# Optimization experiments

Measured on AMD Instinct MI355X. Metric: run time of the kernel, lower is better.

Reference implementation:

```python
import jax, jax.numpy as jnp
import numpy as np

D_MODEL = 1024; D_STATE = 64; D_CONV = 7; EXPAND = 2; HEADDIM = 64; NGROUPS = 1
D_INNER = EXPAND * D_MODEL            # 2048
NHEADS = D_INNER // HEADDIM           # 32
D_IN_PROJ = 2 * D_INNER + 2 * (2 * NGROUPS * D_STATE) + 2 * NHEADS  # 4416
CONV_DIM = D_INNER + 2 * (2 * NGROUPS * D_STATE)                     # 2304
BATCH = 2; SEQLEN = 2048
EPS = 1e-5


def setup_inputs() -> dict:
    key = jax.random.key(0)
    ks = jax.random.split(key, 8)
    u = jax.random.normal(ks[0], (BATCH, SEQLEN, D_MODEL), jnp.float32)
    W_in = jax.random.normal(ks[1], (D_IN_PROJ, D_MODEL), jnp.float32) * 0.02
    conv_w = jax.random.normal(ks[2], (CONV_DIM, 1, D_CONV), jnp.float32) * 0.2
    conv_b = jax.random.normal(ks[3], (CONV_DIM,), jnp.float32) * 0.02
    # dt_bias init as in module: inv-softplus of dt sampled log-uniform in [dt_min, dt_max]
    dt = jnp.exp(jax.random.uniform(ks[4], (NHEADS,)) * (np.log(0.1) - np.log(0.001)) + np.log(0.001))
    dt = jnp.clip(dt, 1e-4)
    dt_bias = dt + jnp.log(-jnp.expm1(-dt))
    A_log = jnp.zeros((NHEADS,), jnp.float32)          # A = -exp(A_log) = -1
    Dp = jnp.ones((NHEADS,), jnp.float32)
    fc_D_w = jax.random.normal(ks[5], (NHEADS, D_INNER), jnp.float32) * 0.02
    norm_w = jnp.ones((D_INNER,), jnp.float32)
    W_out = jax.random.normal(ks[6], (D_MODEL, D_INNER), jnp.float32) * 0.02
    return dict(u=u, W_in=W_in, conv_w=conv_w, conv_b=conv_b, dt_bias=dt_bias,
                A_log=A_log, Dp=Dp, fc_D_w=fc_D_w, norm_w=norm_w, W_out=W_out)


def reference(u, W_in, conv_w, conv_b, dt_bias, A_log, Dp, fc_D_w, norm_w, W_out):
    b, L, _ = u.shape
    gn = NGROUPS * D_STATE
    zxbcdt = jnp.einsum('bld,ed->ble', u, W_in)              # (b,L,4416)
    A = -jnp.exp(A_log)                                       # (H,)
    z = zxbcdt[..., :D_INNER]
    xBC = zxbcdt[..., D_INNER:D_INNER + CONV_DIM]
    dt_raw = zxbcdt[..., D_INNER + CONV_DIM:]                 # (b,L,2H)
    # fwd dt + time-flipped bwd dt stacked along batch -> (2b,L,H)
    dt = jnp.concatenate([dt_raw[..., :NHEADS], dt_raw[..., NHEADS:][:, ::-1]], axis=0)
    dt = jax.nn.softplus(dt + dt_bias)                        # dt_limit=(0,inf): softplus already >= 0
    # depthwise conv1d, 'same' padding
    xc = jnp.transpose(xBC, (0, 2, 1))                        # (b,Cd,L)
    xc = jax.lax.conv_general_dilated(xc, conv_w, (1,), [(D_CONV // 2, D_CONV // 2)],
                                      dimension_numbers=('NCH', 'OIH', 'NCH'),
                                      feature_group_count=CONV_DIM)
    xc = xc + conv_b[None, :, None]
    xBC = jax.nn.silu(jnp.transpose(xc, (0, 2, 1)))           # (b,L,Cd)
    x = xBC[..., :D_INNER]
    BC = xBC[..., D_INNER:]
    x_og = x
    x2 = jnp.concatenate([x, x[:, ::-1]], axis=0)             # (2b,L,d_inner)
    BC2 = jnp.concatenate([BC[..., :2 * gn], BC[..., 2 * gn:][:, ::-1]], axis=0)
    Bm = BC2[..., :gn].reshape(2 * b, L, NGROUPS, D_STATE)
    Cm = BC2[..., gn:].reshape(2 * b, L, NGROUPS, D_STATE)
    x_scan = x2.reshape(2 * b, L, NHEADS, HEADDIM)
    hpg = NHEADS // NGROUPS
    Bh = jnp.repeat(Bm, hpg, axis=2)                          # (2b,L,H,N)
    Ch = jnp.repeat(Cm, hpg, axis=2)

    def step(state, ins):                                     # state: (2b,H,P,N)
        x_t, dt_t, B_t, C_t = ins
        ex = jnp.exp(A[None, :, None, None] * dt_t[:, :, None, None])
        state = state * ex + x_t[..., None] * B_t[:, :, None, :]
        y_t = jnp.sum(state * C_t[:, :, None, :], axis=-1)    # (2b,H,P)
        return state, y_t

    xs = (jnp.moveaxis(x_scan, 1, 0), jnp.moveaxis(dt, 1, 0),
          jnp.moveaxis(Bh, 1, 0), jnp.moveaxis(Ch, 1, 0))
    state0 = jnp.zeros((2 * b, NHEADS, HEADDIM, D_STATE), u.dtype)
    _, ys = jax.lax.scan(step, state0, xs)                    # (L,2b,H,P)
    y = jnp.moveaxis(ys, 0, 1).reshape(2 * b, L, D_INNER)
    # shift_right: drop last step, zero at t=0
    y = jnp.concatenate([jnp.zeros_like(y[:, :1]), y[:, :-1]], axis=1)
    y_fw, y_bw = y[:b], y[b:][:, ::-1]
    diag_heads = jnp.einsum('bld,hd->blh', x_og, fc_D_w) + Dp # fc_D(x_og) with bias D
    diag = jnp.repeat(diag_heads, HEADDIM, axis=-1)           # expand per-head -> d_inner
    y = y_fw + y_bw + x_og * diag
    # RMSNormGated (norm before gate)
    rms = jnp.sqrt(jnp.mean(y * y, axis=-1, keepdims=True) + EPS)
    y = norm_w * (y / rms) * jax.nn.silu(z)
    return jnp.einsum('ble,de->bld', y, W_out)
```

## Files before the change

kernel.cpp:

```cpp
#include <hip/hip_runtime.h>
#include <cstdint>
#include <cstddef>

#define L_SEQ   2048
#define DMODEL  1024
#define DINNER  2048
#define NHEADS_ 32
#define HEADDIM_ 64
#define DSTATE  64
#define CONVDIM 2304
#define DINPROJ 4416
#define DINPROJ_P 4480
#define BATCH_  2
#define EPS_    1e-5f
#define PITCH   72
#define KSPL    8

typedef __attribute__((ext_vector_type(8))) short bf16x8;
typedef __attribute__((ext_vector_type(4))) float f32x4;
typedef unsigned short ushort_t;
typedef unsigned int uint_t;
typedef __attribute__((address_space(3))) unsigned int as3_uint;
typedef __attribute__((address_space(1))) const unsigned int as1_uint;

__device__ __forceinline__ float silu_f(float v) { return v / (1.f + __expf(-v)); }
__device__ __forceinline__ ushort_t f2bf(float f) {
    uint_t u = __float_as_uint(f);
    return (ushort_t)((u + 0x7FFFu + ((u >> 16) & 1u)) >> 16);
}
__device__ __forceinline__ float bf2f(ushort_t u) {
    return __uint_as_float(((uint_t)u) << 16);
}
__device__ __forceinline__ void gload16(const void* g, void* l) {
    __builtin_amdgcn_global_load_lds((as1_uint*)g, (as3_uint*)l, 16, 0, 0);
}

__global__ __launch_bounds__(256)
void cvt_bf16(const float* __restrict__ src, ushort_t* __restrict__ dst) {
    const size_t i4 = (size_t)blockIdx.x * 256 + threadIdx.x;
    float4 v = reinterpret_cast<const float4*>(src)[i4];
    ushort_t* d = dst + i4 * 4;
    d[0] = f2bf(v.x); d[1] = f2bf(v.y); d[2] = f2bf(v.z); d[3] = f2bf(v.w);
}

__global__ __launch_bounds__(256)
void cvt_bf16_pad(const float* __restrict__ src, ushort_t* __restrict__ dst) {
    const size_t i4 = (size_t)blockIdx.x * 256 + threadIdx.x;
    const int row = (int)(i4 / (DMODEL / 4));
    float4 v = make_float4(0.f, 0.f, 0.f, 0.f);
    if (row < DINPROJ) v = reinterpret_cast<const float4*>(src)[i4];
    ushort_t* d = dst + i4 * 4;
    d[0] = f2bf(v.x); d[1] = f2bf(v.y); d[2] = f2bf(v.z); d[3] = f2bf(v.w);
}

__global__ __launch_bounds__(256)
void cvt_fcd(const float* __restrict__ src, ushort_t* __restrict__ dst) {
    const size_t i4 = (size_t)blockIdx.x * 256 + threadIdx.x;
    const int row = (int)(i4 / (DINNER / 4));
    float4 v = make_float4(0.f, 0.f, 0.f, 0.f);
    if (row < NHEADS_) v = reinterpret_cast<const float4*>(src)[i4];
    ushort_t* d = dst + i4 * 4;
    d[0] = f2bf(v.x); d[1] = f2bf(v.y); d[2] = f2bf(v.z); d[3] = f2bf(v.w);
}

template<int BM, int BN, int WGM, int WGN, int FM, int FN, int MODE>
__global__ __launch_bounds__(256)
void gemm_nt_mfma(const ushort_t* __restrict__ A, const ushort_t* __restrict__ B,
                  float* __restrict__ C, ushort_t* __restrict__ Cbf,
                  int M, int N, int K, int lda, int ldb, int nbn) {
    const int nwg = gridDim.x;
    const int orig = blockIdx.x;
    const int xcd = orig & 7, q = nwg >> 3, r = nwg & 7;
    const int wg = ((xcd < r) ? (xcd * (q + 1)) : (r * (q + 1) + (xcd - r) * q)) + (orig >> 3);

    int bm, bn, kbeg, kend, ks = 0;
    if (MODE == 2) {
        bm = (wg / nbn) * BM; bn = 0; ks = wg % nbn;
        kbeg = ks * (K / nbn); kend = kbeg + K / nbn;
    } else {
        bm = (wg / nbn) * BM; bn = (wg % nbn) * BN;
        kbeg = 0; kend = K;
    }

    constexpr int BUFSZ = (BM + BN) * 64;
    constexpr int EPI_B = (MODE == 2) ? 0 : BM * 256;
    constexpr int SMEM_B = (2 * BUFSZ > EPI_B) ? 2 * BUFSZ : EPI_B;
    __shared__ __align__(16) char smem[SMEM_B];

    const int tid = threadIdx.x;
    const int wave = tid >> 6, lane = tid & 63;
    const int wr = wave / WGN, wc = wave % WGN;
    const int fr = lane & 15, kg = lane >> 4;

    constexpr int AI = BM / 64, BI = BN / 64;
    size_t aoff[AI]; int aLds[AI];
#pragma unroll
    for (int pp = 0; pp < AI; ++pp) {
        int p = wave * AI + pp;
        int row = p * 16 + (lane >> 2);
        int c16 = (lane & 3) ^ ((row >> 1) & 3);
        aoff[pp] = (size_t)(bm + row) * lda + c16 * 8;
        aLds[pp] = p * 1024;
    }
    size_t boff[BI]; int bLds[BI];
#pragma unroll
    for (int pp = 0; pp < BI; ++pp) {
        int p = wave * BI + pp;
        int row = p * 16 + (lane >> 2);
        int c16 = (lane & 3) ^ ((row >> 1) & 3);
        boff[pp] = (size_t)(bn + row) * ldb + c16 * 8;
        bLds[pp] = BM * 64 + p * 1024;
    }

    auto stage = [&](int buf, int k0) {
        char* bp = smem + buf * BUFSZ;
#pragma unroll
        for (int pp = 0; pp < AI; ++pp) gload16(&A[aoff[pp] + k0], bp + aLds[pp]);
#pragma unroll
        for (int pp = 0; pp < BI; ++pp) gload16(&B[boff[pp] + k0], bp + bLds[pp]);
    };

    f32x4 acc[FM][FN];
#pragma unroll
    for (int m = 0; m < FM; ++m)
#pragma unroll
        for (int n = 0; n < FN; ++n) acc[m][n] = (f32x4){0.f, 0.f, 0.f, 0.f};

    stage(0, kbeg);
    __syncthreads();

    const int NT = (kend - kbeg) / 32;
    for (int t = 0; t < NT; ++t) {
        const int cur = t & 1;
        if (t + 1 < NT) stage(cur ^ 1, kbeg + (t + 1) * 32);

        const char* bp = smem + cur * BUFSZ;
        bf16x8 af[FM], bfv[FN];
#pragma unroll
        for (int m = 0; m < FM; ++m) {
            int row = wr * FM * 16 + m * 16 + fr;
            af[m] = *reinterpret_cast<const bf16x8*>(bp + row * 64 + ((kg ^ ((row >> 1) & 3)) << 4));
        }
#pragma unroll
        for (int n = 0; n < FN; ++n) {
            int row = wc * FN * 16 + n * 16 + fr;
            bfv[n] = *reinterpret_cast<const bf16x8*>(bp + BM * 64 + row * 64 + ((kg ^ ((row >> 1) & 3)) << 4));
        }
#pragma unroll
        for (int m = 0; m < FM; ++m)
#pragma unroll
            for (int n = 0; n < FN; ++n)
                acc[m][n] = __builtin_amdgcn_mfma_f32_16x16x32_bf16(af[m], bfv[n], acc[m][n], 0, 0, 0);
        __syncthreads();
    }

    const int rg = lane >> 4;
    if (MODE == 2) {
        float* Cp = C + (size_t)ks * M * NHEADS_;
#pragma unroll
        for (int m = 0; m < FM; ++m)
#pragma unroll
            for (int n = 0; n < FN; ++n) {
                int col = wc * FN * 16 + n * 16 + fr;
#pragma unroll
                for (int r = 0; r < 4; ++r) {
                    int rowg = bm + wr * FM * 16 + m * 16 + rg * 4 + r;
                    if (col < NHEADS_) Cp[(size_t)rowg * NHEADS_ + col] = acc[m][n][r];
                }
            }
    } else {
        constexpr int ESZ = (MODE == 1) ? 2 : 4;
        char* ct = smem;
#pragma unroll
        for (int m = 0; m < FM; ++m)
#pragma unroll
            for (int n = 0; n < FN; ++n) {
#pragma unroll
                for (int r = 0; r < 4; ++r) {
                    int lr = wr * FM * 16 + m * 16 + rg * 4 + r;
                    int lc = wc * FN * 16 + n * 16 + fr;
                    int byte = (lr * 256 + lc * ESZ) ^ ((lr & 7) << 4);
                    if (MODE == 1) *reinterpret_cast<ushort_t*>(ct + byte) = f2bf(acc[m][n][r]);
                    else           *reinterpret_cast<float*>(ct + byte) = acc[m][n][r];
                }
            }
        __syncthreads();
        const int lrow = tid >> 4, seg16 = (tid & 15) * 16;
#pragma unroll
        for (int j = 0; j < BM / 16; ++j) {
            int lr = j * 16 + lrow;
            uint4 v = *reinterpret_cast<const uint4*>(ct + ((lr * 256 + seg16) ^ ((lr & 7) << 4)));
            if (MODE == 1)
                *reinterpret_cast<uint4*>(&Cbf[(size_t)(bm + lr) * N + bn + seg16 / 2]) = v;
            else
                *reinterpret_cast<uint4*>(&C[(size_t)(bm + lr) * N + bn + seg16 / 4]) = v;
        }
    }
}

__global__ __launch_bounds__(256)
void conv_kernel(const ushort_t* __restrict__ zxbf, const float* __restrict__ conv_w,
                 const float* __restrict__ conv_b, ushort_t* __restrict__ xBCbf) {
    const int c = blockIdx.x * 256 + threadIdx.x;
    const int t0 = blockIdx.y * 16;
    const int beta = blockIdx.z;
    float w[7];
#pragma unroll
    for (int k = 0; k < 7; ++k) w[k] = conv_w[c * 7 + k];
    const float bias = conv_b[c];
    const ushort_t* in = zxbf + (size_t)beta * L_SEQ * DINPROJ_P + DINNER + c;
    float win[7];
#pragma unroll
    for (int j = 0; j < 6; ++j) {
        int t = t0 - 3 + j;
        win[j] = (t >= 0 && t < L_SEQ) ? bf2f(in[(size_t)t * DINPROJ_P]) : 0.f;
    }
    for (int i = 0; i < 16; ++i) {
        int t = t0 + i;
        int tl = t + 3;
        win[6] = (tl < L_SEQ) ? bf2f(in[(size_t)tl * DINPROJ_P]) : 0.f;
        float acc = bias;
#pragma unroll
        for (int k = 0; k < 7; ++k) acc += win[k] * w[k];
        xBCbf[((size_t)beta * L_SEQ + t) * CONVDIM + c] = f2bf(silu_f(acc));
#pragma unroll
        for (int j = 0; j < 6; ++j) win[j] = win[j + 1];
    }
}

__global__ __launch_bounds__(256)
void dtla_kernel(const ushort_t* __restrict__ zxbf, const float* __restrict__ dt_bias,
                 const float* __restrict__ A_log, float* __restrict__ labuf) {
    const int idx = blockIdx.x * 256 + threadIdx.x;
    const int h   = idx & 31;
    const int tau = (idx >> 5) & (L_SEQ - 1);
    const int bd  = idx >> 16;
    const int dir = bd >> 1, beta = bd & 1;
    const int tt  = dir ? (L_SEQ - 1 - tau) : tau;
    const float dtraw = bf2f(zxbf[((size_t)beta * L_SEQ + tt) * DINPROJ_P + DINNER + CONVDIM + dir * NHEADS_ + h]);
    const float Ah = -__expf(A_log[h]);
    const float dtv = dtraw + dt_bias[h];
    const float sp = (dtv > 15.f) ? dtv : log1pf(__expf(dtv));
    labuf[((size_t)bd * NHEADS_ + h) * L_SEQ + tau] = Ah * sp;
}

__global__ __launch_bounds__(256)
void ssd_chunk_kernel(const ushort_t* __restrict__ xBCbf, const float* __restrict__ labuf,
                      float* __restrict__ Pbuf, float* __restrict__ sdel,
                      ushort_t* __restrict__ yfw, ushort_t* __restrict__ ybw) {
    const int c  = blockIdx.x;
    const int h  = blockIdx.y;
    const int bd = blockIdx.z;
    const int dir = bd >> 1, beta = bd & 1;
    const int tid = threadIdx.x;
    const int wave = tid >> 6, lane = tid & 63;
    const int wr = wave >> 1, wc = wave & 1;
    const int fr = lane & 15, kg = lane >> 4, rg = lane >> 4;

    __shared__ short Bs[64 * PITCH], Cs[64 * PITCH], XTs[64 * PITCH],
                     BTs[64 * PITCH], Ms[64 * PITCH];
    __shared__ float lslds[64];

    const int row = tid >> 2, seg = tid & 3;
    const int tau_r = c * 64 + row;
    const int tt = dir ? (L_SEQ - 1 - tau_r) : tau_r;
    const ushort_t* gbase = xBCbf + ((size_t)beta * L_SEQ + tt) * CONVDIM;

    union U4 { uint4 v; ushort_t s[8]; };
    U4 x0, x1, b0, b1, c0, c1;
    x0.v = *reinterpret_cast<const uint4*>(gbase + h * 64 + seg * 16);
    x1.v = *reinterpret_cast<const uint4*>(gbase + h * 64 + seg * 16 + 8);
    b0.v = *reinterpret_cast<const uint4*>(gbase + DINNER + dir * 128 + seg * 16);
    b1.v = *reinterpret_cast<const uint4*>(gbase + DINNER + dir * 128 + seg * 16 + 8);
    c0.v = *reinterpret_cast<const uint4*>(gbase + DINNER + dir * 128 + 64 + seg * 16);
    c1.v = *reinterpret_cast<const uint4*>(gbase + DINNER + dir * 128 + 64 + seg * 16 + 8);

    *reinterpret_cast<uint4*>(&Bs[row * PITCH + seg * 16])     = b0.v;
    *reinterpret_cast<uint4*>(&Bs[row * PITCH + seg * 16 + 8]) = b1.v;
    *reinterpret_cast<uint4*>(&Cs[row * PITCH + seg * 16])     = c0.v;
    *reinterpret_cast<uint4*>(&Cs[row * PITCH + seg * 16 + 8]) = c1.v;
#pragma unroll
    for (int k = 0; k < 8; ++k) {
        XTs[(seg * 16 + k) * PITCH + row]     = x0.s[k];
        XTs[(seg * 16 + 8 + k) * PITCH + row] = x1.s[k];
    }

    if (tid < 64) {
        float v = labuf[((size_t)bd * NHEADS_ + h) * L_SEQ + c * 64 + tid];
#pragma unroll
        for (int d = 1; d < 64; d <<= 1) {
            float t = __shfl_up(v, d);
            if (lane >= d) v += t;
        }
        lslds[tid] = v;
        Pbuf[((size_t)bd * NHEADS_ + h) * L_SEQ + c * 64 + tid] = __expf(v);
    }
    __syncthreads();

    {
        const float wrow = __expf(lslds[63] - lslds[row]);
#pragma unroll
        for (int k = 0; k < 8; ++k) {
            BTs[(seg * 16 + k) * PITCH + row]     = (short)f2bf(bf2f(b0.s[k]) * wrow);
            BTs[(seg * 16 + 8 + k) * PITCH + row] = (short)f2bf(bf2f(b1.s[k]) * wrow);
        }
    }

    f32x4 accg[2][2];
#pragma unroll
    for (int mi = 0; mi < 2; ++mi)
#pragma unroll
        for (int nj = 0; nj < 2; ++nj) accg[mi][nj] = (f32x4){0.f, 0.f, 0.f, 0.f};
#pragma unroll
    for (int s = 0; s < 2; ++s) {
        int koff = kg * 8 + s * 32;
        bf16x8 af[2], bfv[2];
#pragma unroll
        for (int mi = 0; mi < 2; ++mi)
            af[mi] = *reinterpret_cast<const bf16x8*>(&Cs[(wr * 32 + mi * 16 + fr) * PITCH + koff]);
#pragma unroll
        for (int nj = 0; nj < 2; ++nj)
            bfv[nj] = *reinterpret_cast<const bf16x8*>(&Bs[(wc * 32 + nj * 16 + fr) * PITCH + koff]);
#pragma unroll
        for (int mi = 0; mi < 2; ++mi)
#pragma unroll
            for (int nj = 0; nj < 2; ++nj)
                accg[mi][nj] = __builtin_amdgcn_mfma_f32_16x16x32_bf16(af[mi], bfv[nj], accg[mi][nj], 0, 0, 0);
    }

#pragma unroll
    for (int mi = 0; mi < 2; ++mi)
#pragma unroll
        for (int nj = 0; nj < 2; ++nj) {
            int j = wc * 32 + nj * 16 + fr;
            float lsj = lslds[j];
#pragma unroll
            for (int r = 0; r < 4; ++r) {
                int i = wr * 32 + mi * 16 + rg * 4 + r;
                float v = accg[mi][nj][r];
                v = (i >= j) ? v * __expf(lslds[i] - lsj) : 0.f;
                Ms[i * PITCH + j] = (short)f2bf(v);
            }
        }
    __syncthreads();

    f32x4 accy[2][2], accs[2][2];
#pragma unroll
    for (int mi = 0; mi < 2; ++mi)
#pragma unroll
        for (int nj = 0; nj < 2; ++nj) {
            accy[mi][nj] = (f32x4){0.f, 0.f, 0.f, 0.f};
            accs[mi][nj] = (f32x4){0.f, 0.f, 0.f, 0.f};
        }
#pragma unroll
    for (int s = 0; s < 2; ++s) {
        int koff = kg * 8 + s * 32;
        bf16x8 am[2], axt[2], bxt[2], bbt[2];
#pragma unroll
        for (int mi = 0; mi < 2; ++mi) {
            am[mi]  = *reinterpret_cast<const bf16x8*>(&Ms[(wr * 32 + mi * 16 + fr) * PITCH + koff]);
            axt[mi] = *reinterpret_cast<const bf16x8*>(&XTs[(wr * 32 + mi * 16 + fr) * PITCH + koff]);
        }
#pragma unroll
        for (int nj = 0; nj < 2; ++nj) {
            bxt[nj] = *reinterpret_cast<const bf16x8*>(&XTs[(wc * 32 + nj * 16 + fr) * PITCH + koff]);
            bbt[nj] = *reinterpret_cast<const bf16x8*>(&BTs[(wc * 32 + nj * 16 + fr) * PITCH + koff]);
        }
#pragma unroll
        for (int mi = 0; mi < 2; ++mi)
#pragma unroll
            for (int nj = 0; nj < 2; ++nj) {
                accy[mi][nj] = __builtin_amdgcn_mfma_f32_16x16x32_bf16(am[mi], bxt[nj], accy[mi][nj], 0, 0, 0);
                accs[mi][nj] = __builtin_amdgcn_mfma_f32_16x16x32_bf16(axt[mi], bbt[nj], accs[mi][nj], 0, 0, 0);
            }
    }

    ushort_t* yout = dir ? ybw : yfw;
    float* sd = sdel + ((((size_t)bd * NHEADS_ + h) * 32 + c) * 64) * 64;
#pragma unroll
    for (int mi = 0; mi < 2; ++mi)
#pragma unroll
        for (int nj = 0; nj < 2; ++nj) {
#pragma unroll
            for (int r = 0; r < 4; ++r) {
                int i  = wr * 32 + mi * 16 + rg * 4 + r;
                int jd = wc * 32 + nj * 16 + fr;
                sd[(size_t)i * 64 + jd] = accs[mi][nj][r];
                int tau = c * 64 + i;
                float val = accy[mi][nj][r];
                int tout;
                if (tau == L_SEQ - 1) { tout = dir ? (L_SEQ - 1) : 0; val = 0.f; }
                else                  { tout = dir ? (L_SEQ - 2 - tau) : (tau + 1); }
                yout[((size_t)beta * L_SEQ + tout) * DINNER + h * 64 + jd] = f2bf(val);
            }
        }
}

__global__ __launch_bounds__(256)
void ssd_scan_kernel(const float* __restrict__ Pbuf, float* __restrict__ sdel) {
    const int bh = blockIdx.x;
    const int qt = blockIdx.y;
    const int eo = qt * 1024 + threadIdx.x * 4;
    float* base = sdel + (size_t)bh * 32 * 4096;
    const float* Pb = Pbuf + (size_t)bh * L_SEQ;

    float S0 = 0.f, S1 = 0.f, S2 = 0.f, S3 = 0.f;
    float4 d = *reinterpret_cast<const float4*>(base + eo);
    for (int c = 0; c < 32; ++c) {
        float4 dn;
        if (c + 1 < 32) dn = *reinterpret_cast<const float4*>(base + (size_t)(c + 1) * 4096 + eo);
        const float ptot = Pb[c * 64 + 63];
        *reinterpret_cast<float4*>(base + (size_t)c * 4096 + eo) = make_float4(S0, S1, S2, S3);
        S0 = ptot * S0 + d.x;
        S1 = ptot * S1 + d.y;
        S2 = ptot * S2 + d.z;
        S3 = ptot * S3 + d.w;
        d = dn;
    }
}

__global__ __launch_bounds__(256)
void ssd_yinter_kernel(const ushort_t* __restrict__ xBCbf, const float* __restrict__ Pbuf,
                       const float* __restrict__ sin_buf,
                       ushort_t* __restrict__ yfw, ushort_t* __restrict__ ybw) {
    const int c  = blockIdx.x;
    const int h  = blockIdx.y;
    const int bd = blockIdx.z;
    const int dir = bd >> 1, beta = bd & 1;
    const int tid = threadIdx.x;
    const int wave = tid >> 6, lane = tid & 63;
    const int fr = lane & 15, kg = lane >> 4, rg = lane >> 4;
    const int i0 = wave * 16;

    __shared__ short Cs[64 * PITCH], Ss[64 * PITCH];
    __shared__ float Pl[64];

    const int row = tid >> 2, seg = tid & 3;
    {
        const int tau_r = c * 64 + row;
        const int tt = dir ? (L_SEQ - 1 - tau_r) : tau_r;
        const ushort_t* gbase = xBCbf + ((size_t)beta * L_SEQ + tt) * CONVDIM + DINNER + dir * 128 + 64;
        uint4 cv0 = *reinterpret_cast<const uint4*>(gbase + seg * 16);
        uint4 cv1 = *reinterpret_cast<const uint4*>(gbase + seg * 16 + 8);
        *reinterpret_cast<uint4*>(&Cs[row * PITCH + seg * 16])     = cv0;
        *reinterpret_cast<uint4*>(&Cs[row * PITCH + seg * 16 + 8]) = cv1;
    }
    {
        const float* sb = sin_buf + (((size_t)bd * NHEADS_ + h) * 32 + c) * 4096 + row * 64 + seg * 16;
#pragma unroll
        for (int g = 0; g < 4; ++g) {
            float4 v = *reinterpret_cast<const float4*>(sb + g * 4);
            ushort_t* dst = (ushort_t*)&Ss[row * PITCH + seg * 16 + g * 4];
            dst[0] = f2bf(v.x); dst[1] = f2bf(v.y); dst[2] = f2bf(v.z); dst[3] = f2bf(v.w);
        }
    }
    if (tid < 64) Pl[tid] = Pbuf[((size_t)bd * NHEADS_ + h) * L_SEQ + c * 64 + tid];
    __syncthreads();

    f32x4 accy[4];
#pragma unroll
    for (int nf = 0; nf < 4; ++nf) accy[nf] = (f32x4){0.f, 0.f, 0.f, 0.f};
#pragma unroll
    for (int s = 0; s < 2; ++s) {
        int koff = kg * 8 + s * 32;
        bf16x8 af = *reinterpret_cast<const bf16x8*>(&Cs[(i0 + fr) * PITCH + koff]);
#pragma unroll
        for (int nf = 0; nf < 4; ++nf) {
            bf16x8 bfv = *reinterpret_cast<const bf16x8*>(&Ss[(nf * 16 + fr) * PITCH + koff]);
            accy[nf] = __builtin_amdgcn_mfma_f32_16x16x32_bf16(af, bfv, accy[nf], 0, 0, 0);
        }
    }

    ushort_t* yout = dir ? ybw : yfw;
#pragma unroll
    for (int nf = 0; nf < 4; ++nf) {
        int hdl = nf * 16 + fr;
#pragma unroll
        for (int r = 0; r < 4; ++r) {
            int i = i0 + rg * 4 + r;
            int tau = c * 64 + i;
            if (tau == L_SEQ - 1) continue;
            int tout = dir ? (L_SEQ - 2 - tau) : (tau + 1);
            size_t idx = ((size_t)beta * L_SEQ + tout) * DINNER + h * 64 + hdl;
            yout[idx] = f2bf(accy[nf][r] * Pl[i] + bf2f(yout[idx]));
        }
    }
}

__global__ __launch_bounds__(256)
void combine_rms(const ushort_t* __restrict__ yfw, const ushort_t* __restrict__ ybw,
                 const ushort_t* __restrict__ xBCbf, const float* __restrict__ dpart,
                 const float* __restrict__ Dp,
                 const ushort_t* __restrict__ zxbf, const float* __restrict__ norm_w,
                 ushort_t* __restrict__ ybf) {
    const int row = blockIdx.x;
    const int tid = threadIdx.x;
    union U4 { uint4 v; ushort_t s[8]; };
    U4 yf, yb, xv, zv;
    yf.v = *reinterpret_cast<const uint4*>(yfw + (size_t)row * DINNER + tid * 8);
    yb.v = *reinterpret_cast<const uint4*>(ybw + (size_t)row * DINNER + tid * 8);
    xv.v = *reinterpret_cast<const uint4*>(xBCbf + (size_t)row * CONVDIM + tid * 8);
    zv.v = *reinterpret_cast<const uint4*>(zxbf + (size_t)row * DINPROJ_P + tid * 8);
    const int hh = tid >> 3;
    float dgv = Dp[hh];
#pragma unroll
    for (int ks = 0; ks < KSPL; ++ks)
        dgv += dpart[((size_t)ks * (BATCH_ * L_SEQ) + row) * NHEADS_ + hh];
    float v[8];
    float ss = 0.f;
#pragma unroll
    for (int i = 0; i < 8; ++i) {
        float val = bf2f(yf.s[i]) + bf2f(yb.s[i]) + bf2f(xv.s[i]) * dgv;
        v[i] = val;
        ss += val * val;
    }
    ss += __shfl_xor(ss, 1);  ss += __shfl_xor(ss, 2);  ss += __shfl_xor(ss, 4);
    ss += __shfl_xor(ss, 8);  ss += __shfl_xor(ss, 16); ss += __shfl_xor(ss, 32);
    __shared__ float wsum[4];
    if ((tid & 63) == 0) wsum[tid >> 6] = ss;
    __syncthreads();
    ss = wsum[0] + wsum[1] + wsum[2] + wsum[3];
    const float inv = rsqrtf(ss * (1.f / DINNER) + EPS_);
    U4 outv;
#pragma unroll
    for (int i = 0; i < 8; ++i) {
        int c = tid * 8 + i;
        outv.s[i] = f2bf(norm_w[c] * v[i] * inv * silu_f(bf2f(zv.s[i])));
    }
    *reinterpret_cast<uint4*>(ybf + (size_t)row * DINNER + tid * 8) = outv.v;
}

extern "C" void kernel_launch(void* const* d_in, const int* in_sizes, int n_in,
                              void* d_out, int out_size, void* d_ws, size_t ws_size,
                              hipStream_t stream) {
    const float* u       = (const float*)d_in[0];
    const float* W_in    = (const float*)d_in[1];
    const float* conv_w  = (const float*)d_in[2];
    const float* conv_b  = (const float*)d_in[3];
    const float* dt_bias = (const float*)d_in[4];
    const float* A_log   = (const float*)d_in[5];
    const float* Dp      = (const float*)d_in[6];
    const float* fc_D_w  = (const float*)d_in[7];
    const float* norm_w  = (const float*)d_in[8];
    const float* W_out   = (const float*)d_in[9];
    float* out = (float*)d_out;

    const int ROWS = BATCH_ * L_SEQ;
    ushort_t* zxbf  = (ushort_t*)d_ws;
    ushort_t* xBCbf = zxbf  + (size_t)ROWS * DINPROJ_P;
    ushort_t* yfw   = xBCbf + (size_t)ROWS * CONVDIM;
    ushort_t* ybw   = yfw   + (size_t)ROWS * DINNER;
    float* dpart = (float*)(ybw + (size_t)ROWS * DINNER);
    float* labuf = dpart + (size_t)KSPL * ROWS * NHEADS_;
    float* Pbuf  = labuf + (size_t)4 * NHEADS_ * L_SEQ;
    float* sdel  = Pbuf  + (size_t)4 * NHEADS_ * L_SEQ;
    ushort_t* wobf = (ushort_t*)(sdel + (size_t)4 * NHEADS_ * 32 * 64 * 64);
    ushort_t* fcdbf = wobf + (size_t)DMODEL * DINNER;
    ushort_t* ubf  = fcdbf + (size_t)64 * DINNER;
    ushort_t* wibf = ubf  + (size_t)ROWS * DMODEL;
    ushort_t* ybf  = ubf;

    cvt_bf16<<<(ROWS * DMODEL) / 1024, 256, 0, stream>>>(u, ubf);
    cvt_bf16_pad<<<(DINPROJ_P * DMODEL) / 1024, 256, 0, stream>>>(W_in, wibf);
    cvt_bf16<<<(DMODEL * DINNER) / 1024, 256, 0, stream>>>(W_out, wobf);
    cvt_fcd<<<(64 * DINNER) / 1024, 256, 0, stream>>>(fc_D_w, fcdbf);

    gemm_nt_mfma<128, 128, 2, 2, 4, 4, 1><<<(ROWS / 128) * (DINPROJ_P / 128), 256, 0, stream>>>(
        ubf, wibf, nullptr, zxbf, ROWS, DINPROJ_P, DMODEL, DMODEL, DMODEL, DINPROJ_P / 128);

    dim3 gc(CONVDIM / 256, L_SEQ / 16, BATCH_);
    conv_kernel<<<gc, 256, 0, stream>>>(zxbf, conv_w, conv_b, xBCbf);

    dtla_kernel<<<(4 * L_SEQ * NHEADS_) / 256, 256, 0, stream>>>(zxbf, dt_bias, A_log, labuf);

    dim3 ga(32, NHEADS_, 4);
    ssd_chunk_kernel<<<ga, 256, 0, stream>>>(xBCbf, labuf, Pbuf, sdel, yfw, ybw);

    dim3 gsn(4 * NHEADS_, 4);
    ssd_scan_kernel<<<gsn, 256, 0, stream>>>(Pbuf, sdel);

    dim3 gy(32, NHEADS_, 4);
    ssd_yinter_kernel<<<gy, 256, 0, stream>>>(xBCbf, Pbuf, sdel, yfw, ybw);

    gemm_nt_mfma<64, 64, 2, 2, 2, 2, 2><<<(ROWS / 64) * KSPL, 256, 0, stream>>>(
        xBCbf, fcdbf, dpart, nullptr, ROWS, 64, DINNER, CONVDIM, DINNER, KSPL);

    combine_rms<<<ROWS, 256, 0, stream>>>(yfw, ybw, xBCbf, dpart, Dp, zxbf, norm_w, ybf);

    gemm_nt_mfma<128, 64, 2, 2, 4, 2, 0><<<(ROWS / 128) * (DMODEL / 64), 256, 0, stream>>>(
        ybf, wobf, out, nullptr, ROWS, DMODEL, DINNER, DINNER, DINNER, DMODEL / 64);
}
```

Baseline: 227.0 us.

## Store chunk states in bf16, coalesce y stores via LDS, fuse converts

The four fp32-to-bf16 conversion kernels become one launch, which saves launch overhead. The inter-chunk state buffer is stored in bf16 instead of fp32, halving the traffic for writing it in the chunk kernel and for reading and writing it in the scan and yinter kernels. Outputs of the chunk and yinter kernels are staged through LDS so global stores and read-modify-writes use 16-byte vectors instead of scattered 2-byte accesses. The trade-off is lower precision in the running state, since the scan now reads and writes bf16 each chunk, plus extra syncthreads.

```diff
diff --git a/kernel.cpp b/kernel.cpp
--- a/kernel.cpp
+++ b/kernel.cpp
@@ -35,30 +35,30 @@
     __builtin_amdgcn_global_load_lds((as1_uint*)g, (as3_uint*)l, 16, 0, 0);
 }
 
-__global__ __launch_bounds__(256)
-void cvt_bf16(const float* __restrict__ src, ushort_t* __restrict__ dst) {
-    const size_t i4 = (size_t)blockIdx.x * 256 + threadIdx.x;
-    float4 v = reinterpret_cast<const float4*>(src)[i4];
-    ushort_t* d = dst + i4 * 4;
-    d[0] = f2bf(v.x); d[1] = f2bf(v.y); d[2] = f2bf(v.z); d[3] = f2bf(v.w);
-}
-
-__global__ __launch_bounds__(256)
-void cvt_bf16_pad(const float* __restrict__ src, ushort_t* __restrict__ dst) {
-    const size_t i4 = (size_t)blockIdx.x * 256 + threadIdx.x;
-    const int row = (int)(i4 / (DMODEL / 4));
-    float4 v = make_float4(0.f, 0.f, 0.f, 0.f);
-    if (row < DINPROJ) v = reinterpret_cast<const float4*>(src)[i4];
-    ushort_t* d = dst + i4 * 4;
-    d[0] = f2bf(v.x); d[1] = f2bf(v.y); d[2] = f2bf(v.z); d[3] = f2bf(v.w);
-}
-
-__global__ __launch_bounds__(256)
-void cvt_fcd(const float* __restrict__ src, ushort_t* __restrict__ dst) {
-    const size_t i4 = (size_t)blockIdx.x * 256 + threadIdx.x;
-    const int row = (int)(i4 / (DINNER / 4));
-    float4 v = make_float4(0.f, 0.f, 0.f, 0.f);
-    if (row < NHEADS_) v = reinterpret_cast<const float4*>(src)[i4];
+#define N0U ((size_t)(4096 * 1024 / 4))
+#define N1U ((size_t)(DINPROJ_P * DMODEL / 4))
+#define N2U ((size_t)(DMODEL * DINNER / 4))
+#define N3U ((size_t)(64 * DINNER / 4))
+__global__ __launch_bounds__(256)
+void cvt_all(const float* __restrict__ u, const float* __restrict__ W_in,
+             const float* __restrict__ W_out, const float* __restrict__ fcD,
+             ushort_t* __restrict__ ubf, ushort_t* __restrict__ wibf,
+             ushort_t* __restrict__ wobf, ushort_t* __restrict__ fcdbf) {
+    size_t unit = (size_t)blockIdx.x * 256 + threadIdx.x;
+    const float* src; ushort_t* dst; size_t i4; bool zero = false;
+    if (unit < N0U) {
+        i4 = unit; src = u; dst = ubf;
+    } else if (unit < N0U + N1U) {
+        i4 = unit - N0U; src = W_in; dst = wibf;
+        zero = ((int)(i4 / (DMODEL / 4)) >= DINPROJ);
+    } else if (unit < N0U + N1U + N2U) {
+        i4 = unit - N0U - N1U; src = W_out; dst = wobf;
+    } else {
+        i4 = unit - N0U - N1U - N2U; src = fcD; dst = fcdbf;
+        zero = ((int)(i4 / (DINNER / 4)) >= NHEADS_);
+    }
+    float4 v = zero ? make_float4(0.f, 0.f, 0.f, 0.f)
+                    : reinterpret_cast<const float4*>(src)[i4];
     ushort_t* d = dst + i4 * 4;
     d[0] = f2bf(v.x); d[1] = f2bf(v.y); d[2] = f2bf(v.z); d[3] = f2bf(v.w);
 }
@@ -246,7 +246,7 @@
 
 __global__ __launch_bounds__(256)
 void ssd_chunk_kernel(const ushort_t* __restrict__ xBCbf, const float* __restrict__ labuf,
-                      float* __restrict__ Pbuf, float* __restrict__ sdel,
+                      float* __restrict__ Pbuf, ushort_t* __restrict__ sdel,
                       ushort_t* __restrict__ yfw, ushort_t* __restrict__ ybw) {
     const int c  = blockIdx.x;
     const int h  = blockIdx.y;
@@ -375,8 +375,8 @@
             }
     }
 
-    ushort_t* yout = dir ? ybw : yfw;
-    float* sd = sdel + ((((size_t)bd * NHEADS_ + h) * 32 + c) * 64) * 64;
+    ushort_t* Yt = (ushort_t*)Bs;
+    ushort_t* St = (ushort_t*)Cs;
 #pragma unroll
     for (int mi = 0; mi < 2; ++mi)
 #pragma unroll
@@ -385,43 +385,56 @@
             for (int r = 0; r < 4; ++r) {
                 int i  = wr * 32 + mi * 16 + rg * 4 + r;
                 int jd = wc * 32 + nj * 16 + fr;
-                sd[(size_t)i * 64 + jd] = accs[mi][nj][r];
-                int tau = c * 64 + i;
-                float val = accy[mi][nj][r];
-                int tout;
-                if (tau == L_SEQ - 1) { tout = dir ? (L_SEQ - 1) : 0; val = 0.f; }
-                else                  { tout = dir ? (L_SEQ - 2 - tau) : (tau + 1); }
-                yout[((size_t)beta * L_SEQ + tout) * DINNER + h * 64 + jd] = f2bf(val);
+                St[i * 64 + jd] = f2bf(accs[mi][nj][r]);
+                Yt[i * 64 + jd] = f2bf(accy[mi][nj][r]);
             }
         }
-}
-
-__global__ __launch_bounds__(256)
-void ssd_scan_kernel(const float* __restrict__ Pbuf, float* __restrict__ sdel) {
+    __syncthreads();
+
+    ushort_t* yout = dir ? ybw : yfw;
+    ushort_t* sdp = sdel + (((size_t)bd * NHEADS_ + h) * 32 + c) * 4096;
+    for (int un = tid; un < 512; un += 256) {
+        const int rowi = un >> 3, ch = un & 7;
+        uint4 sv = *reinterpret_cast<const uint4*>(St + rowi * 64 + ch * 8);
+        *reinterpret_cast<uint4*>(sdp + rowi * 64 + ch * 8) = sv;
+        uint4 yv = *reinterpret_cast<const uint4*>(Yt + rowi * 64 + ch * 8);
+        int tau = c * 64 + rowi;
+        int tout;
+        if (tau == L_SEQ - 1) { tout = dir ? (L_SEQ - 1) : 0; yv = make_uint4(0, 0, 0, 0); }
+        else                  { tout = dir ? (L_SEQ - 2 - tau) : (tau + 1); }
+        *reinterpret_cast<uint4*>(yout + ((size_t)beta * L_SEQ + tout) * DINNER + h * 64 + ch * 8) = yv;
+    }
+}
+
+__global__ __launch_bounds__(256)
+void ssd_scan_kernel(const float* __restrict__ Pbuf, ushort_t* __restrict__ sdel) {
     const int bh = blockIdx.x;
     const int qt = blockIdx.y;
     const int eo = qt * 1024 + threadIdx.x * 4;
-    float* base = sdel + (size_t)bh * 32 * 4096;
+    ushort_t* base = sdel + (size_t)bh * 32 * 4096;
     const float* Pb = Pbuf + (size_t)bh * L_SEQ;
 
     float S0 = 0.f, S1 = 0.f, S2 = 0.f, S3 = 0.f;
-    float4 d = *reinterpret_cast<const float4*>(base + eo);
+    uint2 d = *reinterpret_cast<const uint2*>(base + eo);
     for (int c = 0; c < 32; ++c) {
-        float4 dn;
-        if (c + 1 < 32) dn = *reinterpret_cast<const float4*>(base + (size_t)(c + 1) * 4096 + eo);
+        uint2 dn;
+        if (c + 1 < 32) dn = *reinterpret_cast<const uint2*>(base + (size_t)(c + 1) * 4096 + eo);
         const float ptot = Pb[c * 64 + 63];
-        *reinterpret_cast<float4*>(base + (size_t)c * 4096 + eo) = make_float4(S0, S1, S2, S3);
-        S0 = ptot * S0 + d.x;
-        S1 = ptot * S1 + d.y;
-        S2 = ptot * S2 + d.z;
-        S3 = ptot * S3 + d.w;
+        uint2 pv;
+        pv.x = (uint_t)f2bf(S0) | ((uint_t)f2bf(S1) << 16);
+        pv.y = (uint_t)f2bf(S2) | ((uint_t)f2bf(S3) << 16);
+        *reinterpret_cast<uint2*>(base + (size_t)c * 4096 + eo) = pv;
+        S0 = ptot * S0 + bf2f((ushort_t)(d.x & 0xFFFF));
+        S1 = ptot * S1 + bf2f((ushort_t)(d.x >> 16));
+        S2 = ptot * S2 + bf2f((ushort_t)(d.y & 0xFFFF));
+        S3 = ptot * S3 + bf2f((ushort_t)(d.y >> 16));
         d = dn;
     }
 }
 
 __global__ __launch_bounds__(256)
 void ssd_yinter_kernel(const ushort_t* __restrict__ xBCbf, const float* __restrict__ Pbuf,
-                       const float* __restrict__ sin_buf,
+                       const ushort_t* __restrict__ sin_buf,
                        ushort_t* __restrict__ yfw, ushort_t* __restrict__ ybw) {
     const int c  = blockIdx.x;
     const int h  = blockIdx.y;
@@ -446,12 +459,11 @@
         *reinterpret_cast<uint4*>(&Cs[row * PITCH + seg * 16 + 8]) = cv1;
     }
     {
-        const float* sb = sin_buf + (((size_t)bd * NHEADS_ + h) * 32 + c) * 4096 + row * 64 + seg * 16;
-#pragma unroll
-        for (int g = 0; g < 4; ++g) {
-            float4 v = *reinterpret_cast<const float4*>(sb + g * 4);
-            ushort_t* dst = (ushort_t*)&Ss[row * PITCH + seg * 16 + g * 4];
-            dst[0] = f2bf(v.x); dst[1] = f2bf(v.y); dst[2] = f2bf(v.z); dst[3] = f2bf(v.w);
+        const ushort_t* sb = sin_buf + (((size_t)bd * NHEADS_ + h) * 32 + c) * 4096;
+        for (int un = tid; un < 512; un += 256) {
+            const int ri = un >> 3, ch = un & 7;
+            uint4 v = *reinterpret_cast<const uint4*>(sb + ri * 64 + ch * 8);
+            *reinterpret_cast<uint4*>(&Ss[ri * PITCH + ch * 8]) = v;
         }
     }
     if (tid < 64) Pl[tid] = Pbuf[((size_t)bd * NHEADS_ + h) * L_SEQ + c * 64 + tid];
@@ -470,20 +482,33 @@
             accy[nf] = __builtin_amdgcn_mfma_f32_16x16x32_bf16(af, bfv, accy[nf], 0, 0, 0);
         }
     }
-
-    ushort_t* yout = dir ? ybw : yfw;
+    __syncthreads();
+
+    ushort_t* Yt = (ushort_t*)Cs;
 #pragma unroll
     for (int nf = 0; nf < 4; ++nf) {
         int hdl = nf * 16 + fr;
 #pragma unroll
         for (int r = 0; r < 4; ++r) {
             int i = i0 + rg * 4 + r;
-            int tau = c * 64 + i;
-            if (tau == L_SEQ - 1) continue;
-            int tout = dir ? (L_SEQ - 2 - tau) : (tau + 1);
-            size_t idx = ((size_t)beta * L_SEQ + tout) * DINNER + h * 64 + hdl;
-            yout[idx] = f2bf(accy[nf][r] * Pl[i] + bf2f(yout[idx]));
-        }
+            Yt[i * 64 + hdl] = f2bf(accy[nf][r] * Pl[i]);
+        }
+    }
+    __syncthreads();
+
+    ushort_t* yout = dir ? ybw : yfw;
+    for (int un = tid; un < 512; un += 256) {
+        const int ri = un >> 3, ch = un & 7;
+        int tau = c * 64 + ri;
+        if (tau == L_SEQ - 1) continue;
+        int tout = dir ? (L_SEQ - 2 - tau) : (tau + 1);
+        ushort_t* gp = yout + ((size_t)beta * L_SEQ + tout) * DINNER + h * 64 + ch * 8;
+        union U4 { uint4 v; ushort_t s[8]; } yo, cv, res;
+        yo.v = *reinterpret_cast<const uint4*>(gp);
+        cv.v = *reinterpret_cast<const uint4*>(Yt + ri * 64 + ch * 8);
+#pragma unroll
+        for (int k = 0; k < 8; ++k) res.s[k] = f2bf(bf2f(yo.s[k]) + bf2f(cv.s[k]));
+        *reinterpret_cast<uint4*>(gp) = res.v;
     }
 }
 
@@ -553,17 +578,16 @@
     float* dpart = (float*)(ybw + (size_t)ROWS * DINNER);
     float* labuf = dpart + (size_t)KSPL * ROWS * NHEADS_;
     float* Pbuf  = labuf + (size_t)4 * NHEADS_ * L_SEQ;
-    float* sdel  = Pbuf  + (size_t)4 * NHEADS_ * L_SEQ;
-    ushort_t* wobf = (ushort_t*)(sdel + (size_t)4 * NHEADS_ * 32 * 64 * 64);
+    ushort_t* sdel = (ushort_t*)(Pbuf + (size_t)4 * NHEADS_ * L_SEQ);
+    ushort_t* wobf = sdel + (size_t)4 * NHEADS_ * 32 * 64 * 64;
     ushort_t* fcdbf = wobf + (size_t)DMODEL * DINNER;
     ushort_t* ubf  = fcdbf + (size_t)64 * DINNER;
     ushort_t* wibf = ubf  + (size_t)ROWS * DMODEL;
     ushort_t* ybf  = ubf;
 
-    cvt_bf16<<<(ROWS * DMODEL) / 1024, 256, 0, stream>>>(u, ubf);
-    cvt_bf16_pad<<<(DINPROJ_P * DMODEL) / 1024, 256, 0, stream>>>(W_in, wibf);
-    cvt_bf16<<<(DMODEL * DINNER) / 1024, 256, 0, stream>>>(W_out, wobf);
-    cvt_fcd<<<(64 * DINNER) / 1024, 256, 0, stream>>>(fc_D_w, fcdbf);
+    const size_t total_units = N0U + N1U + N2U + N3U;
+    cvt_all<<<(int)((total_units + 255) / 256), 256, 0, stream>>>(
+        u, W_in, W_out, fc_D_w, ubf, wibf, wobf, fcdbf);
 
     gemm_nt_mfma<128, 128, 2, 2, 4, 4, 1><<<(ROWS / 128) * (DINPROJ_P / 128), 256, 0, stream>>>(
         ubf, wibf, nullptr, zxbf, ROWS, DINPROJ_P, DMODEL, DMODEL, DMODEL, DINPROJ_P / 128);
```

Result: faster. 207.3 us (-8.7%).
